# Kernel tuning notes

Measured on AMD Instinct MI355X. Metric: run time of the kernel, lower is better.

Reference implementation:

```python
import jax, jax.numpy as jnp
import numpy as np

H = 768       # hidden_size
NH = 12       # num_attention_heads
HD = H // NH  # head_size
FF = 3072     # intermediate_size
EPS = 1e-5


def _layernorm(x, g, b):
    m = jnp.mean(x, axis=-1, keepdims=True)
    v = jnp.var(x, axis=-1, keepdims=True)
    return (x - m) * jax.lax.rsqrt(v + EPS) * g + b


def setup_inputs() -> dict:
    key = jax.random.key(0)
    ks = jax.random.split(key, 12)
    B, Sq, Skv = 8, 1024, 1024
    s = 0.02
    return {
        "freq_hidden_states": jax.random.normal(ks[0], (B, Sq, H), jnp.float32),
        "image_hidden_states": jax.random.normal(ks[1], (B, Skv, H), jnp.float32),
        # attention projections (stored [in, out])
        "Wq": jax.random.normal(ks[2], (H, H), jnp.float32) * s,
        "bq": jnp.zeros((H,), jnp.float32),
        "Wk": jax.random.normal(ks[3], (H, H), jnp.float32) * s,
        "bk": jnp.zeros((H,), jnp.float32),
        "Wv": jax.random.normal(ks[4], (H, H), jnp.float32) * s,
        "bv": jnp.zeros((H,), jnp.float32),
        # layernorms
        "ln_att_g": jnp.ones((H,), jnp.float32),
        "ln_att_b": jnp.zeros((H,), jnp.float32),
        "ln_mlp_g": jnp.ones((H,), jnp.float32),
        "ln_mlp_b": jnp.zeros((H,), jnp.float32),
        # MLP
        "W1": jax.random.normal(ks[5], (H, FF), jnp.float32) * s,
        "b1": jnp.zeros((FF,), jnp.float32),
        "W2": jax.random.normal(ks[6], (FF, H), jnp.float32) * s,
        "b2": jnp.zeros((H,), jnp.float32),
    }


def reference(image_hidden_states, freq_hidden_states, Wq, bq, Wk, bk, Wv, bv,
              ln_att_g, ln_att_b, ln_mlp_g, ln_mlp_b, W1, b1, W2, b2):
    B, Sq, _ = freq_hidden_states.shape
    Skv = image_hidden_states.shape[1]
    # cross-attention: query from freq, key/value from image
    q = (freq_hidden_states @ Wq + bq).reshape(B, Sq, NH, HD)
    k = (image_hidden_states @ Wk + bk).reshape(B, Skv, NH, HD)
    v = (image_hidden_states @ Wv + bv).reshape(B, Skv, NH, HD)
    scores = jnp.einsum("bqhd,bkhd->bhqk", q, k) / jnp.sqrt(jnp.float32(HD))
    probs = jax.nn.softmax(scores, axis=-1)
    ctx = jnp.einsum("bhqk,bkhd->bqhd", probs, v).reshape(B, Sq, H)
    # residual with post-LN on the attention output
    h = freq_hidden_states + _layernorm(ctx, ln_att_g, ln_att_b)
    # MLP + residual with post-LN on the MLP output
    mlp = jax.nn.relu(h @ W1 + b1) @ W2 + b2
    return h + _layernorm(mlp, ln_mlp_g, ln_mlp_b)
```

## Files before the change

### kernel.cpp

```cpp
#include <hip/hip_runtime.h>
#include <hip/hip_bf16.h>

#define H 768
#define NH 12
#define HD 64
#define FF 3072
#define SQ 1024
#define SKV 1024

typedef __hip_bfloat16 bf16;
typedef __attribute__((ext_vector_type(8))) short short8;
typedef __attribute__((ext_vector_type(4))) float f32x4;

__device__ inline void gload16(const void* g, void* l) {
  __builtin_amdgcn_global_load_lds((const __attribute__((address_space(1))) void*)g,
                                   (__attribute__((address_space(3))) void*)l, 16, 0, 0);
}

__device__ inline float bf2f(unsigned short u) {
  unsigned int x = ((unsigned int)u) << 16;
  return __builtin_bit_cast(float, x);
}

__device__ inline unsigned int cvtpk(float lo, float hi) {
  unsigned int r;
  asm("v_cvt_pk_bf16_f32 %0, %1, %2" : "=v"(r) : "v"(lo), "v"(hi));
  return r;
}

__device__ inline void cvt_body(const float* __restrict__ src, bf16* __restrict__ dst, int blk) {
  int i = blk * 256 + threadIdx.x;
  float4 v = ((const float4*)src)[i];
  union { unsigned short u[4]; uint2 q; } o;
  bf16 t0 = __float2bfloat16(v.x); o.u[0] = *(unsigned short*)&t0;
  bf16 t1 = __float2bfloat16(v.y); o.u[1] = *(unsigned short*)&t1;
  bf16 t2 = __float2bfloat16(v.z); o.u[2] = *(unsigned short*)&t2;
  bf16 t3 = __float2bfloat16(v.w); o.u[3] = *(unsigned short*)&t3;
  ((uint2*)dst)[i] = o.q;
}

__device__ inline void trans_body(const float* __restrict__ src, bf16* __restrict__ dst,
                                  int Kd, int Nd, int blk, float* tile ) {
  int ntx = Nd >> 5;
  int n0 = (blk % ntx) << 5, k0 = (blk / ntx) << 5;
  int tx = threadIdx.x & 31, ty = threadIdx.x >> 5;
#pragma unroll
  for (int i = 0; i < 4; ++i)
    tile[(ty + i * 8) * 33 + tx] = src[(size_t)(k0 + ty + i * 8) * Nd + n0 + tx];
  __syncthreads();
#pragma unroll
  for (int i = 0; i < 4; ++i)
    dst[(size_t)(n0 + ty + i * 8) * Kd + k0 + tx] = __float2bfloat16(tile[tx * 33 + ty + i * 8]);
}

__global__ __launch_bounds__(256) void prep(
    const float* freq, const float* image, bf16* freqb, bf16* imageb,
    const float* Wq, const float* Wk, const float* Wv, const float* W1, const float* W2,
    bf16* WTq, bf16* WTk, bf16* WTv, bf16* W1T, bf16* W2T, int c1) {
  __shared__ float tile[32 * 33];
  int b = blockIdx.x;
  if (b < c1) { cvt_body(freq, freqb, b); return; }
  b -= c1;
  if (b < c1) { cvt_body(image, imageb, b); return; }
  b -= c1;
  const int TQ = (H / 32) * (H / 32);
  const int T1 = (FF / 32) * (H / 32);
  if (b < TQ)            { trans_body(Wq, WTq, H, H, b, tile); return; }
  b -= TQ;
  if (b < TQ)            { trans_body(Wk, WTk, H, H, b, tile); return; }
  b -= TQ;
  if (b < TQ)            { trans_body(Wv, WTv, H, H, b, tile); return; }
  b -= TQ;
  if (b < T1)            { trans_body(W1, W1T, H, FF, b, tile); return; }
  b -= T1;
  trans_body(W2, W2T, FF, H, b, tile);
}

template <int EPI, int BN>
__global__ __launch_bounds__(512) void gemm_bt(
    const bf16* __restrict__ A, const bf16* __restrict__ BT,
    const float* __restrict__ bias0, const float* __restrict__ bias1,
    void* __restrict__ out0, void* __restrict__ out1, int M, int N, int K,
    const bf16* __restrict__ Aq, const bf16* __restrict__ BTq,
    const float* __restrict__ biasq, void* __restrict__ outq) {
  constexpr int JF = BN / 32;
  constexpr int BSI = BN / 64;
  __shared__ __align__(16) bf16 lA[128 * 64];
  __shared__ __align__(16) bf16 lB[BN * 64];
  const int t = threadIdx.x;
  const int lane = t & 63, w = t >> 6;
  const int wr = w >> 1, wc = w & 1;
  const int nwg = gridDim.x;
  int bid = blockIdx.x;
  int logical = ((nwg & 7) == 0) ? ((bid & 7) * (nwg >> 3) + (bid >> 3)) : bid;

  bool isq = false;
  int lg = logical;
  const bf16* Ause = A;
  const bf16* BTuse = BT;
  int nt = N / BN;
  if (EPI == 4) {
    const int nkv = (M >> 7) * (2 * H / BN);
    if (logical >= nkv) {
      isq = true; lg = logical - nkv;
      Ause = Aq; BTuse = BTq; nt = H / BN;
    }
  }
  const int m0 = (lg / nt) << 7;
  const int n0 = (lg % nt) * BN;

  const f32x4 fz = {0.f, 0.f, 0.f, 0.f};
  f32x4 acc[2][JF];
#pragma unroll
  for (int i = 0; i < 2; ++i)
#pragma unroll
    for (int j = 0; j < JF; ++j) acc[i][j] = fz;

  for (int kt = 0; kt < K; kt += 64) {
#pragma unroll
    for (int i = 0; i < 2; ++i) {
      int idx = i * 512 + t;
      int row = idx >> 3;
      int chunk = (idx & 7) ^ (row & 7);
      gload16(Ause + (size_t)(m0 + row) * K + kt + chunk * 8, lA + (size_t)(i * 512 + w * 64) * 8);
    }
#pragma unroll
    for (int i = 0; i < BSI; ++i) {
      int idx = i * 512 + t;
      int row = idx >> 3;
      int chunk = (idx & 7) ^ (row & 7);
      gload16(BTuse + (size_t)(n0 + row) * K + kt + chunk * 8, lB + (size_t)(i * 512 + w * 64) * 8);
    }
    __syncthreads();

    short8 af[2][2], bfv[2][JF];
#pragma unroll
    for (int s = 0; s < 2; ++s) {
#pragma unroll
      for (int i = 0; i < 2; ++i) {
        int ra = wr * 32 + i * 16 + (lane & 15);
        int ca = (s * 4 + (lane >> 4)) ^ (ra & 7);
        af[s][i] = *(const short8*)&lA[ra * 64 + ca * 8];
      }
#pragma unroll
      for (int j = 0; j < JF; ++j) {
        int rb = wc * (BN / 2) + j * 16 + (lane & 15);
        int cb = (s * 4 + (lane >> 4)) ^ (rb & 7);
        bfv[s][j] = *(const short8*)&lB[rb * 64 + cb * 8];
      }
    }
#pragma unroll
    for (int s = 0; s < 2; ++s)
#pragma unroll
      for (int i = 0; i < 2; ++i)
#pragma unroll
        for (int j = 0; j < JF; ++j)
          acc[i][j] = __builtin_amdgcn_mfma_f32_16x16x32_bf16(af[s][i], bfv[s][j], acc[i][j], 0, 0, 0);
    __syncthreads();
  }

#pragma unroll
  for (int i = 0; i < 2; ++i) {
    int mbase = m0 + wr * 32 + i * 16 + ((lane >> 4) << 2);
    int mb = mbase & 1023, bidx = mbase >> 10;
#pragma unroll
    for (int j = 0; j < JF; ++j) {
      int n = n0 + wc * (BN / 2) + j * 16 + (lane & 15);
      if (EPI == 4) {
        if (isq) {
          int hlin = bidx * NH + (n >> 6);
#pragma unroll
          for (int r = 0; r < 4; ++r) {
            float v = (acc[i][j][r] + biasq[n]) * 0.180336880f;
            ((bf16*)outq)[((size_t)hlin * SQ + (mb + r)) * HD + (n & 63)] = __float2bfloat16(v);
          }
        } else {
          int sel = (n >= H);
          int nn = n - (sel ? H : 0);
          int hlin = bidx * NH + (nn >> 6);
          float bsv = (sel ? bias1 : bias0)[nn];
          float v0 = acc[i][j][0] + bsv, v1 = acc[i][j][1] + bsv;
          float v2 = acc[i][j][2] + bsv, v3 = acc[i][j][3] + bsv;
          if (!sel) {
            bf16* kp = (bf16*)out0 + ((size_t)hlin * SKV + mb) * HD + (nn & 63);
            kp[0 * HD] = __float2bfloat16(v0);
            kp[1 * HD] = __float2bfloat16(v1);
            kp[2 * HD] = __float2bfloat16(v2);
            kp[3 * HD] = __float2bfloat16(v3);
          } else {
            uint2 u;
            u.x = cvtpk(v0, v1);
            u.y = cvtpk(v2, v3);
            *(uint2*)((bf16*)out1 + ((size_t)hlin * HD + (nn & 63)) * SKV + mb) = u;
          }
        }
      } else {
#pragma unroll
        for (int r = 0; r < 4; ++r) {
          int m = mbase + r;
          float v = acc[i][j][r] + bias0[n];
          if (EPI == 2) v = fmaxf(v, 0.f);
          ((bf16*)out0)[(size_t)m * N + n] = __float2bfloat16(v);
        }
      }
    }
  }
}

__global__ __launch_bounds__(512, 4) void attn_fwd(
    const bf16* __restrict__ Q,
    const bf16* __restrict__ Kg_,
    const bf16* __restrict__ VT,
    bf16* __restrict__ ctx, int nblk) {
  __shared__ __align__(16) bf16 Ks[2][64 * 64];
  __shared__ __align__(16) bf16 Vs[2][64 * 64];
  __shared__ __align__(16) bf16 PQ[8 * 16 * 72];

  const int t = threadIdx.x, lane = t & 63, w = t >> 6;
  int bid = blockIdx.x;
  int logical = ((nblk & 7) == 0) ? (bid & 7) * (nblk >> 3) + (bid >> 3) : bid;
  const int hl = logical >> 3;
  const int q0 = (logical & 7) << 7;
  const bf16* Qg = Q + ((size_t)hl * SQ + q0) * HD;
  const bf16* Kg = Kg_ + (size_t)hl * SKV * HD;
  const bf16* Vg = VT + (size_t)hl * HD * SKV;

#pragma unroll
  for (int rep = 0; rep < 2; ++rep) {
    int idx = rep * 512 + t;
    int row = idx >> 3;
    int chunk = (idx & 7) ^ (row & 7);
    gload16(Qg + (size_t)row * HD + chunk * 8, PQ + (size_t)(rep * 512 + w * 64) * 8);
  }
  {
    int row = t >> 3, chunk = (t & 7) ^ (row & 7);
    gload16(Kg + (size_t)row * HD + chunk * 8, &Ks[0][(size_t)w * 64 * 8]);
    gload16(Vg + (size_t)row * SKV + chunk * 8, &Vs[0][(size_t)w * 64 * 8]);
  }
  __syncthreads();

  short8 aq[2];
#pragma unroll
  for (int s = 0; s < 2; ++s) {
    int row = w * 16 + (lane & 15);
    int chunk = (s * 4 + (lane >> 4)) ^ (row & 7);
    aq[s] = *(const short8*)&PQ[row * 64 + chunk * 8];
  }
  __syncthreads();

  float l_r[4];
#pragma unroll
  for (int r = 0; r < 4; ++r) l_r[r] = 0.f;
  const f32x4 fz = {0.f, 0.f, 0.f, 0.f};
  f32x4 oacc[4];
#pragma unroll
  for (int j = 0; j < 4; ++j) oacc[j] = fz;

  bf16* Pw = PQ + w * (16 * 72);
  const short s1 = (short)0x3F80;
  const short8 ones = {s1, s1, s1, s1, s1, s1, s1, s1};

#pragma unroll 2
  for (int i = 0; i < 16; ++i) {
    const int buf = i & 1;
    if (i < 15) {
      int kvn = (i + 1) << 6;
      int row = t >> 3, chunk = (t & 7) ^ (row & 7);
      gload16(Kg + (size_t)(kvn + row) * HD + chunk * 8, &Ks[buf ^ 1][(size_t)w * 64 * 8]);
      gload16(Vg + (size_t)row * SKV + kvn + chunk * 8, &Vs[buf ^ 1][(size_t)w * 64 * 8]);
    }

    f32x4 sa[4];
#pragma unroll
    for (int n = 0; n < 4; ++n) sa[n] = fz;
    __builtin_amdgcn_s_setprio(1);
#pragma unroll
    for (int s = 0; s < 2; ++s)
#pragma unroll
      for (int n = 0; n < 4; ++n) {
        int rb = n * 16 + (lane & 15);
        int cb = (s * 4 + (lane >> 4)) ^ (rb & 7);
        short8 bk = *(const short8*)&Ks[buf][rb * 64 + cb * 8];
        sa[n] = __builtin_amdgcn_mfma_f32_16x16x32_bf16(bk, aq[s], sa[n], 0, 0, 0);
      }
    __builtin_amdgcn_s_setprio(0);

#pragma unroll
    for (int n = 0; n < 4; ++n) {
      uint2 pk2;
      pk2.x = cvtpk(exp2f(sa[n][0]), exp2f(sa[n][1]));
      pk2.y = cvtpk(exp2f(sa[n][2]), exp2f(sa[n][3]));
      *(uint2*)&Pw[(lane & 15) * 72 + n * 16 + ((lane >> 4) << 2)] = pk2;
    }

    f32x4 ld = fz;
    __builtin_amdgcn_s_setprio(1);
#pragma unroll
    for (int kk = 0; kk < 2; ++kk) {
      short8 pa = *(const short8*)&Pw[(lane & 15) * 72 + kk * 32 + ((lane >> 4) << 3)];
      ld = __builtin_amdgcn_mfma_f32_16x16x32_bf16(pa, ones, ld, 0, 0, 0);
#pragma unroll
      for (int j = 0; j < 4; ++j) {
        int rb = j * 16 + (lane & 15);
        int cb = (kk * 4 + (lane >> 4)) ^ (rb & 7);
        short8 bv = *(const short8*)&Vs[buf][rb * 64 + cb * 8];
        oacc[j] = __builtin_amdgcn_mfma_f32_16x16x32_bf16(pa, bv, oacc[j], 0, 0, 0);
      }
    }
    __builtin_amdgcn_s_setprio(0);
#pragma unroll
    for (int r = 0; r < 4; ++r) l_r[r] += ld[r];

    __syncthreads();
  }

  const int b = hl / NH, hh = hl % NH;
  float rl[4];
#pragma unroll
  for (int r = 0; r < 4; ++r) rl[r] = 1.0f / l_r[r];
#pragma unroll
  for (int j = 0; j < 4; ++j)
#pragma unroll
    for (int r = 0; r < 4; ++r) {
      int q = q0 + w * 16 + ((lane >> 4) << 2) + r;
      int d = j * 16 + (lane & 15);
      ctx[((size_t)b * SQ + q) * H + hh * HD + d] = __float2bfloat16(oacc[j][r] * rl[r]);
    }
}

__global__ __launch_bounds__(192) void ln_res(
    const bf16* __restrict__ x, const bf16* __restrict__ res,
    const float* __restrict__ g, const float* __restrict__ beta,
    float* __restrict__ o32, bf16* __restrict__ ob) {
  const int row = blockIdx.x;
  const int t = threadIdx.x;
  float v[4];
  float s = 0.f, s2 = 0.f;
  ushort4 xv = ((const ushort4*)(x + (size_t)row * H))[t];
  v[0] = bf2f(xv.x); v[1] = bf2f(xv.y); v[2] = bf2f(xv.z); v[3] = bf2f(xv.w);
#pragma unroll
  for (int k = 0; k < 4; ++k) { s += v[k]; s2 += v[k] * v[k]; }
#pragma unroll
  for (int off = 32; off > 0; off >>= 1) {
    s += __shfl_down(s, off);
    s2 += __shfl_down(s2, off);
  }
  __shared__ float red[8];
  if ((t & 63) == 0) { red[t >> 6] = s; red[4 + (t >> 6)] = s2; }
  __syncthreads();
  float st = red[0] + red[1] + red[2];
  float s2t = red[4] + red[5] + red[6];
  float mean = st * (1.f / 768.f);
  float var = s2t * (1.f / 768.f) - mean * mean;
  float rs = rsqrtf(var + 1e-5f);
  {
    ushort4 rv4 = ((const ushort4*)(res + (size_t)row * H))[t];
    float4 gv = ((const float4*)g)[t];
    float4 bv = ((const float4*)beta)[t];
    float4 o;
    o.x = bf2f(rv4.x) + (v[0] - mean) * rs * gv.x + bv.x;
    o.y = bf2f(rv4.y) + (v[1] - mean) * rs * gv.y + bv.y;
    o.z = bf2f(rv4.z) + (v[2] - mean) * rs * gv.z + bv.z;
    o.w = bf2f(rv4.w) + (v[3] - mean) * rs * gv.w + bv.w;
    if (o32) ((float4*)(o32 + (size_t)row * H))[t] = o;
    if (ob) {
      uint2 q;
      q.x = cvtpk(o.x, o.y);
      q.y = cvtpk(o.z, o.w);
      ((uint2*)(ob + (size_t)row * H))[t] = q;
    }
  }
}

extern "C" void kernel_launch(void* const* d_in, const int* in_sizes, int n_in,
                              void* d_out, int out_size, void* d_ws, size_t ws_size,
                              hipStream_t stream) {
  const float* freq  = (const float*)d_in[0];
  const float* image = (const float*)d_in[1];
  const float* Wq = (const float*)d_in[2];
  const float* bq = (const float*)d_in[3];
  const float* Wk = (const float*)d_in[4];
  const float* bk = (const float*)d_in[5];
  const float* Wv = (const float*)d_in[6];
  const float* bv = (const float*)d_in[7];
  const float* g1 = (const float*)d_in[8];
  const float* be1 = (const float*)d_in[9];
  const float* g2 = (const float*)d_in[10];
  const float* be2 = (const float*)d_in[11];
  const float* W1 = (const float*)d_in[12];
  const float* b1 = (const float*)d_in[13];
  const float* W2 = (const float*)d_in[14];
  const float* b2 = (const float*)d_in[15];

  const int Bc = in_sizes[0] / (SQ * H);
  const int M = Bc * SQ;

  char* p = (char*)d_ws;
  bf16* W1T = (bf16*)p;  p += (size_t)FF * H * 2;
  bf16* W2T = (bf16*)p;  p += (size_t)H * FF * 2;
  bf16* ctxb = (bf16*)p; p += (size_t)M * H * 2;
  bf16* hb = (bf16*)p;   p += (size_t)M * H * 2;
  char* U = p;
  bf16* freqb = (bf16*)U;
  bf16* imageb = (bf16*)(U + (size_t)M * H * 2);
  bf16* WTq   = (bf16*)(U + (size_t)2 * M * H * 2);
  bf16* WTkv  = (bf16*)(U + (size_t)2 * M * H * 2 + (size_t)H * H * 2);
  bf16* Qb    = (bf16*)(U + (size_t)2 * M * H * 2 + (size_t)3 * H * H * 2);
  bf16* Kbuf  = (bf16*)((char*)Qb + (size_t)M * H * 2);
  bf16* VTb   = (bf16*)((char*)Kbuf + (size_t)M * H * 2);
  bf16* mlp1  = (bf16*)U;
  bf16* mlp2b = ctxb;

  int c1 = M * H / 1024;
  int nprep = 2 * c1 + 3 * ((H / 32) * (H / 32)) + (FF / 32) * (H / 32) + (H / 32) * (FF / 32);
  prep<<<nprep, 256, 0, stream>>>(freq, image, freqb, imageb,
                                  Wq, Wk, Wv, W1, W2,
                                  WTq, WTkv, WTkv + (size_t)H * H, W1T, W2T, c1);

  int nqkv = (M / 128) * (2 * H / 128) + (M / 128) * (H / 128);
  gemm_bt<4, 128><<<nqkv, 512, 0, stream>>>(imageb, WTkv, bk, bv, Kbuf, VTb, M, 2 * H, H,
                                            freqb, WTq, bq, Qb);
  int nblk = Bc * NH * (SQ / 128);
  attn_fwd<<<nblk, 512, 0, stream>>>(Qb, Kbuf, VTb, ctxb, nblk);
  ln_res<<<M, 192, 0, stream>>>(ctxb, freqb, g1, be1, nullptr, hb);
  gemm_bt<2, 128><<<(M / 128) * (FF / 128), 512, 0, stream>>>(hb, W1T, b1, nullptr, mlp1, nullptr,
                                                              M, FF, H, nullptr, nullptr, nullptr, nullptr);
  gemm_bt<3, 64><<<(M / 128) * (H / 64), 512, 0, stream>>>(mlp1, W2T, b2, nullptr, mlp2b, nullptr,
                                                           M, H, FF, nullptr, nullptr, nullptr, nullptr);
  ln_res<<<M, 192, 0, stream>>>(mlp2b, hb, g2, be2, (float*)d_out, nullptr);
}
```

Baseline: 217.3 us.

## Split-K the MLP down-projection and swizzle the attention P buffer

The second MLP GEMM (K=3072, N=768) now runs as a two-way split-K launch with twice as many workgroups. Each half writes unbiased bf16 partial sums to its own buffer, and the following layernorm kernel adds the two partials and the bias before normalising. Separately, the attention kernel's per-wave probability buffer drops its 72-element row padding for an XOR-swizzled 64-wide layout, which cuts LDS use and aims to avoid bank conflicts. The split adds an extra M×H bf16 write and read, and each partial is rounded to bf16 before the sum, which slightly changes precision.

Result: slower. 226.8 us (+4.4%).

```diff
diff --git a/kernel.cpp b/kernel.cpp
--- a/kernel.cpp
+++ b/kernel.cpp
@@ -95,10 +95,12 @@
   int logical = ((nwg & 7) == 0) ? ((bid & 7) * (nwg >> 3) + (bid >> 3)) : bid;
 
   bool isq = false;
+  int ksplit = 0;
   int lg = logical;
   const bf16* Ause = A;
   const bf16* BTuse = BT;
   int nt = N / BN;
+  int koff = 0, kend = K;
   if (EPI == 4) {
     const int nkv = (M >> 7) * (2 * H / BN);
     if (logical >= nkv) {
@@ -106,6 +108,13 @@
       Ause = Aq; BTuse = BTq; nt = H / BN;
     }
   }
+  if (EPI == 5) {
+    const int ntiles = (M >> 7) * (N / BN);
+    ksplit = (lg >= ntiles);
+    lg -= ksplit * ntiles;
+    koff = ksplit * (K >> 1);
+    kend = koff + (K >> 1);
+  }
   const int m0 = (lg / nt) << 7;
   const int n0 = (lg % nt) * BN;
 
@@ -116,7 +125,7 @@
 #pragma unroll
     for (int j = 0; j < JF; ++j) acc[i][j] = fz;
 
-  for (int kt = 0; kt < K; kt += 64) {
+  for (int kt = koff; kt < kend; kt += 64) {
 #pragma unroll
     for (int i = 0; i < 2; ++i) {
       int idx = i * 512 + t;
@@ -194,6 +203,13 @@
             *(uint2*)((bf16*)out1 + ((size_t)hlin * HD + (nn & 63)) * SKV + mb) = u;
           }
         }
+      } else if (EPI == 5) {
+        bf16* po = (bf16*)(ksplit ? out1 : out0);
+#pragma unroll
+        for (int r = 0; r < 4; ++r) {
+          int m = mbase + r;
+          po[(size_t)m * N + n] = __float2bfloat16(acc[i][j][r]);
+        }
       } else {
 #pragma unroll
         for (int r = 0; r < 4; ++r) {
@@ -214,7 +230,7 @@
     bf16* __restrict__ ctx, int nblk) {
   __shared__ __align__(16) bf16 Ks[2][64 * 64];
   __shared__ __align__(16) bf16 Vs[2][64 * 64];
-  __shared__ __align__(16) bf16 PQ[8 * 16 * 72];
+  __shared__ __align__(16) bf16 PQ[8 * 16 * 64];
 
   const int t = threadIdx.x, lane = t & 63, w = t >> 6;
   int bid = blockIdx.x;
@@ -256,7 +272,7 @@
 #pragma unroll
   for (int j = 0; j < 4; ++j) oacc[j] = fz;
 
-  bf16* Pw = PQ + w * (16 * 72);
+  bf16* Pw = PQ + w * (16 * 64);
   const short s1 = (short)0x3F80;
   const short8 ones = {s1, s1, s1, s1, s1, s1, s1, s1};
 
@@ -290,14 +306,16 @@
       uint2 pk2;
       pk2.x = cvtpk(exp2f(sa[n][0]), exp2f(sa[n][1]));
       pk2.y = cvtpk(exp2f(sa[n][2]), exp2f(sa[n][3]));
-      *(uint2*)&Pw[(lane & 15) * 72 + n * 16 + ((lane >> 4) << 2)] = pk2;
+      int cs = (n * 2 + ((lane >> 4) >> 1)) ^ (lane & 7);
+      *(uint2*)&Pw[(lane & 15) * 64 + cs * 8 + ((lane >> 4) & 1) * 4] = pk2;
     }
 
     f32x4 ld = fz;
     __builtin_amdgcn_s_setprio(1);
 #pragma unroll
     for (int kk = 0; kk < 2; ++kk) {
-      short8 pa = *(const short8*)&Pw[(lane & 15) * 72 + kk * 32 + ((lane >> 4) << 3)];
+      int cp = (kk * 4 + (lane >> 4)) ^ (lane & 7);
+      short8 pa = *(const short8*)&Pw[(lane & 15) * 64 + cp * 8];
       ld = __builtin_amdgcn_mfma_f32_16x16x32_bf16(pa, ones, ld, 0, 0, 0);
 #pragma unroll
       for (int j = 0; j < 4; ++j) {
@@ -329,7 +347,8 @@
 }
 
 __global__ __launch_bounds__(192) void ln_res(
-    const bf16* __restrict__ x, const bf16* __restrict__ res,
+    const bf16* __restrict__ x, const bf16* __restrict__ x2, const float* __restrict__ bias,
+    const bf16* __restrict__ res,
     const float* __restrict__ g, const float* __restrict__ beta,
     float* __restrict__ o32, bf16* __restrict__ ob) {
   const int row = blockIdx.x;
@@ -338,6 +357,14 @@
   float s = 0.f, s2 = 0.f;
   ushort4 xv = ((const ushort4*)(x + (size_t)row * H))[t];
   v[0] = bf2f(xv.x); v[1] = bf2f(xv.y); v[2] = bf2f(xv.z); v[3] = bf2f(xv.w);
+  if (x2) {
+    ushort4 y = ((const ushort4*)(x2 + (size_t)row * H))[t];
+    v[0] += bf2f(y.x); v[1] += bf2f(y.y); v[2] += bf2f(y.z); v[3] += bf2f(y.w);
+  }
+  if (bias) {
+    float4 b4 = ((const float4*)bias)[t];
+    v[0] += b4.x; v[1] += b4.y; v[2] += b4.z; v[3] += b4.w;
+  }
 #pragma unroll
   for (int k = 0; k < 4; ++k) { s += v[k]; s2 += v[k] * v[k]; }
 #pragma unroll
@@ -409,7 +436,8 @@
   bf16* Kbuf  = (bf16*)((char*)Qb + (size_t)M * H * 2);
   bf16* VTb   = (bf16*)((char*)Kbuf + (size_t)M * H * 2);
   bf16* mlp1  = (bf16*)U;
-  bf16* mlp2b = ctxb;
+  bf16* mlp2a = ctxb;
+  bf16* mlp2b = VTb;
 
   int c1 = M * H / 1024;
   int nprep = 2 * c1 + 3 * ((H / 32) * (H / 32)) + (FF / 32) * (H / 32) + (H / 32) * (FF / 32);
@@ -422,10 +450,10 @@
                                             freqb, WTq, bq, Qb);
   int nblk = Bc * NH * (SQ / 128);
   attn_fwd<<<nblk, 512, 0, stream>>>(Qb, Kbuf, VTb, ctxb, nblk);
-  ln_res<<<M, 192, 0, stream>>>(ctxb, freqb, g1, be1, nullptr, hb);
+  ln_res<<<M, 192, 0, stream>>>(ctxb, nullptr, nullptr, freqb, g1, be1, nullptr, hb);
   gemm_bt<2, 128><<<(M / 128) * (FF / 128), 512, 0, stream>>>(hb, W1T, b1, nullptr, mlp1, nullptr,
                                                               M, FF, H, nullptr, nullptr, nullptr, nullptr);
-  gemm_bt<3, 64><<<(M / 128) * (H / 64), 512, 0, stream>>>(mlp1, W2T, b2, nullptr, mlp2b, nullptr,
-                                                           M, H, FF, nullptr, nullptr, nullptr, nullptr);
-  ln_res<<<M, 192, 0, stream>>>(mlp2b, hb, g2, be2, (float*)d_out, nullptr);
-}
+  gemm_bt<5, 64><<<2 * (M / 128) * (H / 64), 512, 0, stream>>>(mlp1, W2T, nullptr, nullptr, mlp2a, mlp2b,
+                                                               M, H, FF, nullptr, nullptr, nullptr, nullptr);
+  ln_res<<<M, 192, 0, stream>>>(mlp2a, mlp2b, b2, hb, g2, be2, (float*)d_out, nullptr);
+}
```

## Rewrite attention inner loop with 32x32x16 MFMA and register-resident P

Applied to the files above, without the earlier changes.

Switches the attention kernel from 16x16x32 MFMAs to 32x32x16 MFMAs. Each pair of waves shares a 32-query group and splits the KV tile between them, then reduces partial outputs and row sums through LDS at the end. Probabilities are now repacked in registers with permlane32_swap instead of being stored to LDS and reloaded, and the row sum is computed with scalar adds instead of an extra MFMA against a ones vector. Q is loaded directly into registers. The intent is to cut LDS traffic and MFMA instruction count, at the cost of a cross-wave reduction and a different occupancy hint.

Result: no change. 216.1 us (-0.5%).

```diff
diff --git a/kernel.cpp b/kernel.cpp
--- a/kernel.cpp
+++ b/kernel.cpp
@@ -11,6 +11,7 @@
 typedef __hip_bfloat16 bf16;
 typedef __attribute__((ext_vector_type(8))) short short8;
 typedef __attribute__((ext_vector_type(4))) float f32x4;
+typedef __attribute__((ext_vector_type(16))) float f32x16;
 
 __device__ inline void gload16(const void* g, void* l) {
   __builtin_amdgcn_global_load_lds((const __attribute__((address_space(1))) void*)g,
@@ -207,16 +208,18 @@
   }
 }
 
-__global__ __launch_bounds__(512, 4) void attn_fwd(
+__global__ __launch_bounds__(512) void attn_fwd(
     const bf16* __restrict__ Q,
     const bf16* __restrict__ Kg_,
     const bf16* __restrict__ VT,
     bf16* __restrict__ ctx, int nblk) {
-  __shared__ __align__(16) bf16 Ks[2][64 * 64];
-  __shared__ __align__(16) bf16 Vs[2][64 * 64];
-  __shared__ __align__(16) bf16 PQ[8 * 16 * 72];
+  __shared__ __align__(16) bf16 Kb[2][64 * 64];
+  __shared__ __align__(16) bf16 Vb[2][64 * 64];
+  __shared__ float Lsum[4][32];
 
   const int t = threadIdx.x, lane = t & 63, w = t >> 6;
+  const int hi = lane >> 5, l31 = lane & 31;
+  const int qg = w >> 1, h = w & 1;
   int bid = blockIdx.x;
   int logical = ((nblk & 7) == 0) ? (bid & 7) * (nblk >> 3) + (bid >> 3) : bid;
   const int hl = logical >> 3;
@@ -225,40 +228,25 @@
   const bf16* Kg = Kg_ + (size_t)hl * SKV * HD;
   const bf16* Vg = VT + (size_t)hl * HD * SKV;
 
-#pragma unroll
-  for (int rep = 0; rep < 2; ++rep) {
-    int idx = rep * 512 + t;
-    int row = idx >> 3;
-    int chunk = (idx & 7) ^ (row & 7);
-    gload16(Qg + (size_t)row * HD + chunk * 8, PQ + (size_t)(rep * 512 + w * 64) * 8);
-  }
+  short8 aq[4];
+  {
+    const bf16* qp = Qg + (size_t)(qg * 32 + l31) * HD;
+#pragma unroll
+    for (int ks = 0; ks < 4; ++ks)
+      aq[ks] = *(const short8*)(qp + (ks * 2 + hi) * 8);
+  }
+
   {
     int row = t >> 3, chunk = (t & 7) ^ (row & 7);
-    gload16(Kg + (size_t)row * HD + chunk * 8, &Ks[0][(size_t)w * 64 * 8]);
-    gload16(Vg + (size_t)row * SKV + chunk * 8, &Vs[0][(size_t)w * 64 * 8]);
+    gload16(Kg + (size_t)row * HD + chunk * 8, (char*)&Kb[0][0] + (size_t)t * 16);
+    gload16(Vg + (size_t)row * SKV + chunk * 8, (char*)&Vb[0][0] + (size_t)t * 16);
   }
   __syncthreads();
 
-  short8 aq[2];
-#pragma unroll
-  for (int s = 0; s < 2; ++s) {
-    int row = w * 16 + (lane & 15);
-    int chunk = (s * 4 + (lane >> 4)) ^ (row & 7);
-    aq[s] = *(const short8*)&PQ[row * 64 + chunk * 8];
-  }
-  __syncthreads();
-
-  float l_r[4];
-#pragma unroll
-  for (int r = 0; r < 4; ++r) l_r[r] = 0.f;
-  const f32x4 fz = {0.f, 0.f, 0.f, 0.f};
-  f32x4 oacc[4];
-#pragma unroll
-  for (int j = 0; j < 4; ++j) oacc[j] = fz;
-
-  bf16* Pw = PQ + w * (16 * 72);
-  const short s1 = (short)0x3F80;
-  const short8 ones = {s1, s1, s1, s1, s1, s1, s1, s1};
+  f32x16 oa0, oa1;
+#pragma unroll
+  for (int r = 0; r < 16; ++r) { oa0[r] = 0.f; oa1[r] = 0.f; }
+  float lacc = 0.f;
 
 #pragma unroll 2
   for (int i = 0; i < 16; ++i) {
@@ -266,66 +254,86 @@
     if (i < 15) {
       int kvn = (i + 1) << 6;
       int row = t >> 3, chunk = (t & 7) ^ (row & 7);
-      gload16(Kg + (size_t)(kvn + row) * HD + chunk * 8, &Ks[buf ^ 1][(size_t)w * 64 * 8]);
-      gload16(Vg + (size_t)row * SKV + kvn + chunk * 8, &Vs[buf ^ 1][(size_t)w * 64 * 8]);
-    }
-
-    f32x4 sa[4];
-#pragma unroll
-    for (int n = 0; n < 4; ++n) sa[n] = fz;
+      gload16(Kg + (size_t)(kvn + row) * HD + chunk * 8, (char*)&Kb[buf ^ 1][0] + (size_t)t * 16);
+      gload16(Vg + (size_t)row * SKV + kvn + chunk * 8, (char*)&Vb[buf ^ 1][0] + (size_t)t * 16);
+    }
+
+    f32x16 sc;
+#pragma unroll
+    for (int r = 0; r < 16; ++r) sc[r] = 0.f;
     __builtin_amdgcn_s_setprio(1);
 #pragma unroll
-    for (int s = 0; s < 2; ++s)
-#pragma unroll
-      for (int n = 0; n < 4; ++n) {
-        int rb = n * 16 + (lane & 15);
-        int cb = (s * 4 + (lane >> 4)) ^ (rb & 7);
-        short8 bk = *(const short8*)&Ks[buf][rb * 64 + cb * 8];
-        sa[n] = __builtin_amdgcn_mfma_f32_16x16x32_bf16(bk, aq[s], sa[n], 0, 0, 0);
-      }
+    for (int ks = 0; ks < 4; ++ks) {
+      int c0 = ks * 2 + hi;
+      int r0 = h * 32 + l31;
+      short8 kf = *(const short8*)&Kb[buf][r0 * 64 + ((c0 ^ (r0 & 7)) * 8)];
+      sc = __builtin_amdgcn_mfma_f32_32x32x16_bf16(kf, aq[ks], sc, 0, 0, 0);
+    }
     __builtin_amdgcn_s_setprio(0);
 
 #pragma unroll
-    for (int n = 0; n < 4; ++n) {
-      uint2 pk2;
-      pk2.x = cvtpk(exp2f(sa[n][0]), exp2f(sa[n][1]));
-      pk2.y = cvtpk(exp2f(sa[n][2]), exp2f(sa[n][3]));
-      *(uint2*)&Pw[(lane & 15) * 72 + n * 16 + ((lane >> 4) << 2)] = pk2;
-    }
-
-    f32x4 ld = fz;
+    for (int r = 0; r < 16; ++r) { sc[r] = exp2f(sc[r]); lacc += sc[r]; }
+
+    short8 pa[2];
+#pragma unroll
+    for (int k4 = 0; k4 < 2; ++k4) {
+      const int base = k4 * 8;
+      unsigned int p0 = cvtpk(sc[base + 0], sc[base + 1]);
+      unsigned int p1 = cvtpk(sc[base + 2], sc[base + 3]);
+      unsigned int qq0 = cvtpk(sc[base + 4], sc[base + 5]);
+      unsigned int qq1 = cvtpk(sc[base + 6], sc[base + 7]);
+      asm volatile("v_permlane32_swap_b32 %0, %1" : "+v"(p0), "+v"(qq0));
+      asm volatile("v_permlane32_swap_b32 %0, %1" : "+v"(p1), "+v"(qq1));
+      union { unsigned int u[4]; short8 s8; } pu;
+      pu.u[0] = p0; pu.u[1] = p1; pu.u[2] = qq0; pu.u[3] = qq1;
+      pa[k4] = pu.s8;
+    }
+
     __builtin_amdgcn_s_setprio(1);
 #pragma unroll
-    for (int kk = 0; kk < 2; ++kk) {
-      short8 pa = *(const short8*)&Pw[(lane & 15) * 72 + kk * 32 + ((lane >> 4) << 3)];
-      ld = __builtin_amdgcn_mfma_f32_16x16x32_bf16(pa, ones, ld, 0, 0, 0);
-#pragma unroll
-      for (int j = 0; j < 4; ++j) {
-        int rb = j * 16 + (lane & 15);
-        int cb = (kk * 4 + (lane >> 4)) ^ (rb & 7);
-        short8 bv = *(const short8*)&Vs[buf][rb * 64 + cb * 8];
-        oacc[j] = __builtin_amdgcn_mfma_f32_16x16x32_bf16(pa, bv, oacc[j], 0, 0, 0);
-      }
+    for (int k4 = 0; k4 < 2; ++k4) {
+      int cc = 4 * h + k4 * 2 + hi;
+      int r0 = l31;
+      short8 vf0 = *(const short8*)&Vb[buf][r0 * 64 + ((cc ^ (r0 & 7)) * 8)];
+      oa0 = __builtin_amdgcn_mfma_f32_32x32x16_bf16(pa[k4], vf0, oa0, 0, 0, 0);
+      int r1 = 32 + l31;
+      short8 vf1 = *(const short8*)&Vb[buf][r1 * 64 + ((cc ^ (r1 & 7)) * 8)];
+      oa1 = __builtin_amdgcn_mfma_f32_32x32x16_bf16(pa[k4], vf1, oa1, 0, 0, 0);
     }
     __builtin_amdgcn_s_setprio(0);
-#pragma unroll
-    for (int r = 0; r < 4; ++r) l_r[r] += ld[r];
 
     __syncthreads();
   }
 
-  const int b = hl / NH, hh = hl % NH;
-  float rl[4];
-#pragma unroll
-  for (int r = 0; r < 4; ++r) rl[r] = 1.0f / l_r[r];
-#pragma unroll
-  for (int j = 0; j < 4; ++j)
-#pragma unroll
-    for (int r = 0; r < 4; ++r) {
-      int q = q0 + w * 16 + ((lane >> 4) << 2) + r;
-      int d = j * 16 + (lane & 15);
-      ctx[((size_t)b * SQ + q) * H + hh * HD + d] = __float2bfloat16(oacc[j][r] * rl[r]);
-    }
+  float lt = lacc + __shfl_xor(lacc, 32);
+
+  float* Cg = (qg < 2) ? ((float*)&Kb[0][0] + qg * 2048)
+                       : ((float*)&Vb[0][0] + (qg - 2) * 2048);
+  if (h == 1) {
+#pragma unroll
+    for (int r = 0; r < 16; ++r) {
+      int ro = (r & 3) + 8 * (r >> 2) + 4 * hi;
+      Cg[ro * 64 + l31] = oa0[r];
+      Cg[ro * 64 + 32 + l31] = oa1[r];
+    }
+    if (hi == 0) Lsum[qg][l31] = lt;
+  }
+  __syncthreads();
+  if (h == 0) {
+    float rlq = 1.0f / (lt + Lsum[qg][l31]);
+    const int b = hl / NH, hh = hl % NH;
+    bf16* outp = ctx + ((size_t)b * SQ + q0 + qg * 32) * H + hh * HD;
+#pragma unroll
+    for (int r = 0; r < 16; ++r) {
+      int qo = (r & 3) + 8 * (r >> 2) + 4 * hi;
+      float rv = __shfl(rlq, qo);
+      float v0 = oa0[r] + Cg[qo * 64 + l31];
+      float v1 = oa1[r] + Cg[qo * 64 + 32 + l31];
+      bf16* rowp = outp + (size_t)qo * H;
+      rowp[l31]      = __float2bfloat16(v0 * rv);
+      rowp[32 + l31] = __float2bfloat16(v1 * rv);
+    }
+  }
 }
 
 __global__ __launch_bounds__(192) void ln_res(
```
